# Optimization experiments

Measured on AMD Instinct MI355X. Metric: run time of the kernel, lower is better.

The kernel has to match this reference:

```python
import jax, jax.numpy as jnp
import numpy as np

N, E, H, G = 20000, 320000, 256, 128
FN, FE, OUT = 64, 16, 10
EPS_GEN = 1e-7
EPS_BN = 1e-5
EPS_IN = 1e-5


def _lstm_cell_c(x, W, b):
    # torch LSTMCell with zero (h0, c0); only cell state c' is used:
    # c' = sigmoid(i) * tanh(g).  W: [4H, F], gate order i, f, g, o.
    z = x @ W.T + b
    i, f, g, o = jnp.split(z, 4, axis=1)
    return jax.nn.sigmoid(i) * jnp.tanh(g)


def _segment_softmax(scores, seg, num):
    m = jax.ops.segment_max(scores, seg, num_segments=num)
    m = jnp.where(jnp.isfinite(m), m, 0.0)
    e = jnp.exp(scores - m[seg])
    s = jax.ops.segment_sum(e, seg, num_segments=num)
    return e / (s[seg] + 1e-16)


def _gen_conv(x, src, dst, edge_attr, t, w1, b1, gamma, beta, w2, b2):
    # GENConv (aggr='softmax', t learnable scalar, eps=1e-7, 2-layer MLP)
    msg = jax.nn.relu(x[src] + edge_attr) + EPS_GEN          # [E, H]
    alpha = _segment_softmax(msg * t, dst, N)                 # [E, H]
    aggr = jax.ops.segment_sum(alpha * msg, dst, num_segments=N)  # [N, H]
    h = x + aggr
    h = h @ w1.T + b1                                         # [N, 2H]
    # BatchNorm1d in eval mode (running_mean=0, running_var=1)
    h = h / jnp.sqrt(1.0 + EPS_BN) * gamma + beta
    h = jax.nn.relu(h)
    return h @ w2.T + b2                                      # [N, H]


def _instance_norm(x, batch):
    ones = jnp.ones((x.shape[0],), x.dtype)
    cnt = jnp.maximum(jax.ops.segment_sum(ones, batch, num_segments=G), 1.0)[:, None]
    mean = jax.ops.segment_sum(x, batch, num_segments=G) / cnt
    var = jax.ops.segment_sum(x * x, batch, num_segments=G) / cnt - mean ** 2
    return (x - mean[batch]) / jnp.sqrt(var[batch] + EPS_IN)


def setup_inputs() -> dict:
    key = jax.random.key(0)
    ks = jax.random.split(key, 24)

    def glorot(k, shape):
        lim = 1.0 / np.sqrt(shape[-1])
        return jax.random.uniform(k, shape, jnp.float32, -lim, lim)

    inp = {
        "x": jax.random.normal(ks[0], (N, FN), jnp.float32),
        "edge_index": jax.random.randint(ks[1], (2, E), 0, N),
        "edge_attr": jax.random.normal(ks[2], (E, FE), jnp.float32),
        "batch": jnp.sort(jax.random.randint(ks[3], (N,), 0, G)),
        # LSTMCell embeddings
        "node_W": glorot(ks[4], (4 * H, FN)),
        "node_b": glorot(ks[5], (4 * H,)),
        "edge_W": glorot(ks[6], (4 * H, FE)),
        "edge_b": glorot(ks[7], (4 * H,)),
        # GENConv 1
        "t1": jnp.float32(1.0),
        "g1_w1": glorot(ks[8], (2 * H, H)),
        "g1_b1": glorot(ks[9], (2 * H,)),
        "g1_gamma": jnp.ones((2 * H,), jnp.float32),
        "g1_beta": jnp.zeros((2 * H,), jnp.float32),
        "g1_w2": glorot(ks[10], (H, 2 * H)),
        "g1_b2": glorot(ks[11], (H,)),
        # GENConv 2
        "t2": jnp.float32(1.0),
        "g2_w1": glorot(ks[12], (2 * H, H)),
        "g2_b1": glorot(ks[13], (2 * H,)),
        "g2_gamma": jnp.ones((2 * H,), jnp.float32),
        "g2_beta": jnp.zeros((2 * H,), jnp.float32),
        "g2_w2": glorot(ks[14], (H, 2 * H)),
        "g2_b2": glorot(ks[15], (H,)),
        # output Linear
        "lin_w": glorot(ks[16], (OUT, H)),
        "lin_b": glorot(ks[17], (OUT,)),
    }
    return inp


def reference(x, edge_index, edge_attr, batch,
              node_W, node_b, edge_W, edge_b,
              t1, g1_w1, g1_b1, g1_gamma, g1_beta, g1_w2, g1_b2,
              t2, g2_w1, g2_b1, g2_gamma, g2_beta, g2_w2, g2_b2,
              lin_w, lin_b):
    src, dst = edge_index[0], edge_index[1]
    h = _lstm_cell_c(x, node_W, node_b)            # [N, H]
    ea = _lstm_cell_c(edge_attr, edge_W, edge_b)   # [E, H]
    h = jax.nn.relu(_gen_conv(h, src, dst, ea, t1, g1_w1, g1_b1, g1_gamma, g1_beta, g1_w2, g1_b2))
    h = _instance_norm(h, batch)
    h = jax.nn.relu(_gen_conv(h, src, dst, ea, t2, g2_w1, g2_b1, g2_gamma, g2_beta, g2_w2, g2_b2))
    h = _instance_norm(h, batch)
    pooled = jax.ops.segment_max(h, batch, num_segments=G)  # [G, H]
    pooled = jnp.where(jnp.isfinite(pooled), pooled, 0.0)
    # dropout is identity in eval mode
    out = pooled @ lin_w.T + lin_b
    return jax.nn.sigmoid(out)
```

## Files before the change

### kernel.cpp

```cpp
#include <hip/hip_runtime.h>
#include <hip/hip_bf16.h>
#include <math.h>

#define N_NODES 20000
#define N_EDGES 320000
#define HH      256
#define GG      128
#define FN      64
#define FE      16

__device__ __forceinline__ float fast_rcp(float x) {
    return __builtin_amdgcn_rcpf(x);
}
__device__ __forceinline__ float fast_sigmoid(float x) {
    return fast_rcp(1.f + __expf(-x));
}
__device__ __forceinline__ float sig_tanh(float zi, float zg) {
    float u = __expf(-zi);
    float v = __expf(2.f * zg);
    return (v - 1.f) * fast_rcp((1.f + u) * (v + 1.f));
}

__global__ void hist_k(const int* __restrict__ dst, int* __restrict__ cnt) {
    int e = blockIdx.x * blockDim.x + threadIdx.x;
    if (e < N_EDGES) atomicAdd(&cnt[dst[e]], 1);
}

__global__ __launch_bounds__(256) void scan1_k(const int* __restrict__ cnt,
                                               int* __restrict__ ex,
                                               int* __restrict__ bsum) {
    int b = blockIdx.x, t = threadIdx.x;
    int i = b * 256 + t;
    int v = (i < N_NODES) ? cnt[i] : 0;
    int lane = t & 63, w = t >> 6;
    int incl = v;
#pragma unroll
    for (int off = 1; off < 64; off <<= 1) {
        int u = __shfl_up(incl, off);
        if (lane >= off) incl += u;
    }
    __shared__ int wsum[4];
    if (lane == 63) wsum[w] = incl;
    __syncthreads();
    int woff = 0;
#pragma unroll
    for (int j = 0; j < 4; ++j)
        if (j < w) woff += wsum[j];
    if (i < N_NODES) ex[i] = woff + incl - v;
    if (t == 255) bsum[b] = woff + incl;
}

__global__ __launch_bounds__(128) void scan2_k(int* __restrict__ bsum, int nb) {
    int t = threadIdx.x;
    int v = (t < nb) ? bsum[t] : 0;
    int lane = t & 63, w = t >> 6;
    int incl = v;
#pragma unroll
    for (int off = 1; off < 64; off <<= 1) {
        int u = __shfl_up(incl, off);
        if (lane >= off) incl += u;
    }
    __shared__ int wsum[2];
    if (lane == 63) wsum[w] = incl;
    __syncthreads();
    int woff = (w == 1) ? wsum[0] : 0;
    if (t < nb) bsum[t] = woff + incl - v;
}

__global__ __launch_bounds__(256) void scan3_k(const int* __restrict__ cnt,
                                               const int* __restrict__ bsum,
                                               int* __restrict__ rowst,
                                               int* __restrict__ cursor) {
    int b = blockIdx.x, t = threadIdx.x;
    int i = b * 256 + t;
    if (i < N_NODES) {
        int v = rowst[i] + bsum[b];
        rowst[i] = v;
        cursor[i] = v;
        if (i == N_NODES - 1) rowst[N_NODES] = v + cnt[i];
    }
}

__global__ void scatter_k(const int* __restrict__ src,
                          const int* __restrict__ dst,
                          const float* __restrict__ eattr,
                          int* __restrict__ cursor, int* __restrict__ srcs,
                          float* __restrict__ eattrs) {
    int e = blockIdx.x * blockDim.x + threadIdx.x;
    if (e < N_EDGES) {
        int pos = atomicAdd(&cursor[dst[e]], 1);
        srcs[pos] = src[e];
        const float4* a = (const float4*)(eattr + (size_t)e * FE);
        float4* o = (float4*)(eattrs + (size_t)pos * FE);
        o[0] = a[0];
        o[1] = a[1];
        o[2] = a[2];
        o[3] = a[3];
    }
}

__global__ void repack_k(const float* __restrict__ W, const float* __restrict__ b,
                         float* __restrict__ W2, float* __restrict__ b2, int K) {
    int idx = blockIdx.x * blockDim.x + threadIdx.x;
    if (idx < 512 * K) {
        int r = idx / K, k = idx - r * K;
        int c = r >> 1;
        int rs = (r & 1) ? (512 + c) : c;
        W2[idx] = W[rs * K + k];
    } else if (idx < 512 * K + 512) {
        int r = idx - 512 * K;
        int c = r >> 1;
        int rs = (r & 1) ? (512 + c) : c;
        b2[r] = b[rs];
    }
}

#define NPB 8
__global__ __launch_bounds__(256, 8) void genconv_edge_k(
    const float* __restrict__ hin, const __hip_bfloat16* __restrict__ eacsr,
    const int* __restrict__ srcs, const int* __restrict__ rowst,
    const float* __restrict__ tptr, float* __restrict__ aout) {
    int tid = threadIdx.x;
    float tscale = tptr[0];
    int n0 = blockIdx.x * NPB;
    for (int u = 0; u < NPB; ++u) {
        int n = n0 + u;
        if (n >= N_NODES) break;
        int s0 = rowst[n], s1 = rowst[n + 1];
        float hself = hin[(size_t)n * HH + tid];
        float accE0 = 0.f, accWE0 = 0.f, accE1 = 0.f, accWE1 = 0.f;
        int j = s0;
        for (; j + 1 < s1; j += 2) {
            int sn0 = srcs[j], sn1 = srcs[j + 1];
            float ea0 = __bfloat162float(eacsr[(size_t)j * HH + tid]);
            float ea1 = __bfloat162float(eacsr[(size_t)(j + 1) * HH + tid]);
            float h0v = hin[(size_t)sn0 * HH + tid];
            float h1v = hin[(size_t)sn1 * HH + tid];
            float m0 = fmaxf(h0v + ea0, 0.f) + 1e-7f;
            float m1 = fmaxf(h1v + ea1, 0.f) + 1e-7f;
            float p0 = __expf(tscale * m0);
            float p1 = __expf(tscale * m1);
            accE0 += p0;
            accWE0 += p0 * m0;
            accE1 += p1;
            accWE1 += p1 * m1;
        }
        if (j < s1) {
            int sn = srcs[j];
            float eav = __bfloat162float(eacsr[(size_t)j * HH + tid]);
            float hv = hin[(size_t)sn * HH + tid];
            float m0 = fmaxf(hv + eav, 0.f) + 1e-7f;
            float p0 = __expf(tscale * m0);
            accE0 += p0;
            accWE0 += p0 * m0;
        }
        float accE = accE0 + accE1, accWE = accWE0 + accWE1;
        aout[(size_t)n * HH + tid] = hself + accWE / (accE + 1e-16f);
    }
}

#define TM 128
#define TN 128
#define KB 16
__global__ __launch_bounds__(256, 2) void gemm_nt_k(
    const float* __restrict__ A, const float* __restrict__ B,
    const float* __restrict__ bias, const float* __restrict__ gamma,
    const float* __restrict__ beta, float* __restrict__ C, int M, int NN,
    int K, int mode) {
    __shared__ float As[KB][TM + 4];
    __shared__ float Bs[KB][TN + 4];
    int tid = threadIdx.x;
    int row0 = blockIdx.x * TM, col0 = blockIdx.y * TN;
    int tx = tid & 15, ty = tid >> 4;
    int lr = tid >> 2;
    int lc = (tid & 3) * 4;
    float4 va[2], vb[2];
#pragma unroll
    for (int h = 0; h < 2; ++h) {
        int r = lr + h * 64;
        int gr = row0 + r;
        va[h] = (gr < M) ? *(const float4*)&A[(size_t)gr * K + lc]
                         : make_float4(0.f, 0.f, 0.f, 0.f);
        vb[h] = *(const float4*)&B[(size_t)(col0 + r) * K + lc];
    }
    float acc[8][8] = {{0.f}};
    for (int k0 = 0; k0 < K; k0 += KB) {
#pragma unroll
        for (int h = 0; h < 2; ++h) {
            int r = lr + h * 64;
            As[lc + 0][r] = va[h].x;
            As[lc + 1][r] = va[h].y;
            As[lc + 2][r] = va[h].z;
            As[lc + 3][r] = va[h].w;
            Bs[lc + 0][r] = vb[h].x;
            Bs[lc + 1][r] = vb[h].y;
            Bs[lc + 2][r] = vb[h].z;
            Bs[lc + 3][r] = vb[h].w;
        }
        __syncthreads();
        int k1 = k0 + KB;
        if (k1 < K) {
#pragma unroll
            for (int h = 0; h < 2; ++h) {
                int r = lr + h * 64;
                int gr = row0 + r;
                va[h] = (gr < M)
                            ? *(const float4*)&A[(size_t)gr * K + k1 + lc]
                            : make_float4(0.f, 0.f, 0.f, 0.f);
                vb[h] = *(const float4*)&B[(size_t)(col0 + r) * K + k1 + lc];
            }
        }
#pragma unroll
        for (int k = 0; k < KB; ++k) {
            float4 a0 = *(const float4*)&As[k][ty * 4];
            float4 a1 = *(const float4*)&As[k][64 + ty * 4];
            float4 b0 = *(const float4*)&Bs[k][tx * 4];
            float4 b1 = *(const float4*)&Bs[k][64 + tx * 4];
            float av[8] = {a0.x, a0.y, a0.z, a0.w, a1.x, a1.y, a1.z, a1.w};
            float bv[8] = {b0.x, b0.y, b0.z, b0.w, b1.x, b1.y, b1.z, b1.w};
#pragma unroll
            for (int i = 0; i < 8; ++i)
#pragma unroll
                for (int j = 0; j < 8; ++j) acc[i][j] += av[i] * bv[j];
        }
        __syncthreads();
    }
    const float bn_rs = rsqrtf(1.f + 1e-5f);
#pragma unroll
    for (int gj = 0; gj < 2; ++gj) {
        int nb = col0 + gj * 64 + tx * 4;
        float bs[4], sc[4], sh[4];
#pragma unroll
        for (int j = 0; j < 4; ++j) {
            bs[j] = bias[nb + j];
            if (mode == 0) {
                sc[j] = gamma[nb + j] * bn_rs;
                sh[j] = beta[nb + j];
            }
        }
#pragma unroll
        for (int gi = 0; gi < 2; ++gi) {
#pragma unroll
            for (int i2 = 0; i2 < 4; ++i2) {
                int m = row0 + gi * 64 + ty * 4 + i2;
                if (m >= M) continue;
                int i = gi * 4 + i2;
                float y[4];
#pragma unroll
                for (int j = 0; j < 4; ++j) {
                    float v = acc[i][gj * 4 + j] + bs[j];
                    if (mode == 0) v = v * sc[j] + sh[j];
                    if (mode == 0 || mode == 1) v = fmaxf(v, 0.f);
                    y[j] = v;
                }
                if (mode == 3) {
                    float2 o;
                    o.x = sig_tanh(y[0], y[1]);
                    o.y = sig_tanh(y[2], y[3]);
                    *(float2*)&C[(size_t)m * (NN / 2) + nb / 2] = o;
                } else if (mode == 4) {
                    __hip_bfloat162 o;
                    o.x = __float2bfloat16(sig_tanh(y[0], y[1]));
                    o.y = __float2bfloat16(sig_tanh(y[2], y[3]));
                    *(__hip_bfloat162*)((__hip_bfloat16*)C +
                                        (size_t)m * (NN / 2) + nb / 2) = o;
                } else {
                    float4 o = {y[0], y[1], y[2], y[3]};
                    *(float4*)&C[(size_t)m * NN + nb] = o;
                }
            }
        }
    }
}

__device__ __forceinline__ int lowerb(const int* a, int n, int key) {
    int lo = 0, hi = n;
    while (lo < hi) {
        int mid = (lo + hi) >> 1;
        if (a[mid] < key) lo = mid + 1;
        else hi = mid;
    }
    return lo;
}

__global__ __launch_bounds__(256) void inst_norm_k(
    const float* __restrict__ x, const int* __restrict__ batch,
    float* __restrict__ y) {
    __shared__ int sS, sE;
    int g = blockIdx.x, t = threadIdx.x;
    if (t == 0) {
        sS = lowerb(batch, N_NODES, g);
        sE = lowerb(batch, N_NODES, g + 1);
    }
    __syncthreads();
    int s = sS, e = sE;
    float sum = 0.f, ss = 0.f;
    for (int n = s; n < e; ++n) {
        float v = x[(size_t)n * HH + t];
        sum += v;
        ss += v * v;
    }
    float c = (float)((e - s) > 0 ? (e - s) : 1);
    float mean = sum / c;
    float var = ss / c - mean * mean;
    float inv = rsqrtf(var + 1e-5f);
    for (int n = s; n < e; ++n) {
        float v = x[(size_t)n * HH + t];
        y[(size_t)n * HH + t] = (v - mean) * inv;
    }
}

__global__ __launch_bounds__(256) void inpool_k(
    const float* __restrict__ x, const int* __restrict__ batch,
    const float* __restrict__ lw, const float* __restrict__ lb,
    float* __restrict__ out) {
    __shared__ float pooled[HH];
    __shared__ int sS, sE;
    int g = blockIdx.x, t = threadIdx.x;
    if (t == 0) {
        sS = lowerb(batch, N_NODES, g);
        sE = lowerb(batch, N_NODES, g + 1);
    }
    __syncthreads();
    int s = sS, e = sE;
    float sum = 0.f, ss = 0.f;
    for (int n = s; n < e; ++n) {
        float v = x[(size_t)n * HH + t];
        sum += v;
        ss += v * v;
    }
    float c = (float)((e - s) > 0 ? (e - s) : 1);
    float mean = sum / c;
    float var = ss / c - mean * mean;
    float inv = rsqrtf(var + 1e-5f);
    float m = -3.0e38f;
    for (int n = s; n < e; ++n) {
        float v = (x[(size_t)n * HH + t] - mean) * inv;
        m = fmaxf(m, v);
    }
    pooled[t] = (e > s) ? m : 0.f;
    __syncthreads();
    if (t < 10) {
        float acc = lb[t];
        for (int k = 0; k < HH; ++k) acc += pooled[k] * lw[t * HH + k];
        out[g * 10 + t] = fast_sigmoid(acc);
    }
}

extern "C" void kernel_launch(void* const* d_in, const int* in_sizes, int n_in,
                              void* d_out, int out_size, void* d_ws,
                              size_t ws_size, hipStream_t stream) {
    const float* x      = (const float*)d_in[0];
    const int*   ei     = (const int*)d_in[1];
    const float* eattr  = (const float*)d_in[2];
    const int*   batch  = (const int*)d_in[3];
    const float* nodeW  = (const float*)d_in[4];
    const float* nodeb  = (const float*)d_in[5];
    const float* edgeW  = (const float*)d_in[6];
    const float* edgeb  = (const float*)d_in[7];
    const float* t1     = (const float*)d_in[8];
    const float* g1w1   = (const float*)d_in[9];
    const float* g1b1   = (const float*)d_in[10];
    const float* g1g    = (const float*)d_in[11];
    const float* g1be   = (const float*)d_in[12];
    const float* g1w2   = (const float*)d_in[13];
    const float* g1b2   = (const float*)d_in[14];
    const float* t2     = (const float*)d_in[15];
    const float* g2w1   = (const float*)d_in[16];
    const float* g2b1   = (const float*)d_in[17];
    const float* g2g    = (const float*)d_in[18];
    const float* g2be   = (const float*)d_in[19];
    const float* g2w2   = (const float*)d_in[20];
    const float* g2b2   = (const float*)d_in[21];
    const float* linw   = (const float*)d_in[22];
    const float* linb   = (const float*)d_in[23];
    float* out = (float*)d_out;

    const int* srcA = ei;
    const int* dstA = ei + N_EDGES;

    float* F0  = (float*)d_ws;
    float* F1  = F0 + (size_t)N_NODES * HH;
    float* F2  = F1 + (size_t)N_NODES * HH;
    float* W2n = F2 + (size_t)N_NODES * 2 * HH;
    float* b2n = W2n + 512 * 64;
    float* W2e = b2n + 512;
    float* b2e = W2e + 512 * 16;
    float* eattrs = b2e + 512;
    __hip_bfloat16* eacsr =
        (__hip_bfloat16*)(eattrs + (size_t)N_EDGES * FE);
    int* cnt    = (int*)(eacsr + (size_t)N_EDGES * HH);
    int* cursor = cnt + N_NODES;
    int* rowst  = cursor + N_NODES;
    int* srcs   = rowst + N_NODES + 1;
    int* bsum   = srcs + N_EDGES;

    const int NSCB = (N_NODES + 255) / 256;

    hipMemsetAsync(cnt, 0, N_NODES * sizeof(int), stream);
    hist_k<<<(N_EDGES + 255) / 256, 256, 0, stream>>>(dstA, cnt);
    scan1_k<<<NSCB, 256, 0, stream>>>(cnt, rowst, bsum);
    scan2_k<<<1, 128, 0, stream>>>(bsum, NSCB);
    scan3_k<<<NSCB, 256, 0, stream>>>(cnt, bsum, rowst, cursor);
    scatter_k<<<(N_EDGES + 255) / 256, 256, 0, stream>>>(srcA, dstA, eattr,
                                                         cursor, srcs, eattrs);

    repack_k<<<(512 * 64 + 512 + 255) / 256, 256, 0, stream>>>(nodeW, nodeb,
                                                               W2n, b2n, 64);
    repack_k<<<(512 * 16 + 512 + 255) / 256, 256, 0, stream>>>(edgeW, edgeb,
                                                               W2e, b2e, 16);

    dim3 gemm_grid1((N_NODES + TM - 1) / TM, 512 / TN);
    dim3 gemm_grid2((N_NODES + TM - 1) / TM, 256 / TN);

    gemm_nt_k<<<gemm_grid1, 256, 0, stream>>>(x, W2n, b2n, nullptr, nullptr,
                                              F0, N_NODES, 512, 64, 3);
    gemm_nt_k<<<dim3(N_EDGES / TM, 512 / TN), 256, 0, stream>>>(
        eattrs, W2e, b2e, nullptr, nullptr, (float*)eacsr, N_EDGES, 512, 16, 4);

    genconv_edge_k<<<(N_NODES + NPB - 1) / NPB, 256, 0, stream>>>(
        F0, eacsr, srcs, rowst, t1, F1);
    gemm_nt_k<<<gemm_grid1, 256, 0, stream>>>(F1, g1w1, g1b1, g1g, g1be, F2,
                                              N_NODES, 512, 256, 0);
    gemm_nt_k<<<gemm_grid2, 256, 0, stream>>>(F2, g1w2, g1b2, nullptr, nullptr,
                                              F1, N_NODES, 256, 512, 1);
    inst_norm_k<<<GG, 256, 0, stream>>>(F1, batch, F0);

    genconv_edge_k<<<(N_NODES + NPB - 1) / NPB, 256, 0, stream>>>(
        F0, eacsr, srcs, rowst, t2, F1);
    gemm_nt_k<<<gemm_grid1, 256, 0, stream>>>(F1, g2w1, g2b1, g2g, g2be, F2,
                                              N_NODES, 512, 256, 0);
    gemm_nt_k<<<gemm_grid2, 256, 0, stream>>>(F2, g2w2, g2b2, nullptr, nullptr,
                                              F1, N_NODES, 256, 512, 1);

    inpool_k<<<GG, 256, 0, stream>>>(F1, batch, linw, linb, out);
}
```

Before: 978.7 us.

## Move GENConv MLP and edge LSTM GEMMs to split-bf16 MFMA

```diff
diff --git a/kernel.cpp b/kernel.cpp
--- a/kernel.cpp
+++ b/kernel.cpp
@@ -1,13 +1,16 @@
 #include <hip/hip_runtime.h>
-#include <hip/hip_bf16.h>
 #include <math.h>
 
 #define N_NODES 20000
 #define N_EDGES 320000
 #define HH      256
 #define GG      128
-#define FN      64
 #define FE      16
+#define MPAD    20032
+
+typedef short  bf16x8 __attribute__((ext_vector_type(8)));
+typedef float  f32x4  __attribute__((ext_vector_type(4)));
+typedef unsigned short ushort_t;
 
 __device__ __forceinline__ float fast_rcp(float x) {
     return __builtin_amdgcn_rcpf(x);
@@ -19,6 +22,13 @@
     float u = __expf(-zi);
     float v = __expf(2.f * zg);
     return (v - 1.f) * fast_rcp((1.f + u) * (v + 1.f));
+}
+__device__ __forceinline__ ushort_t f2bf(float x) {
+    unsigned u = __float_as_uint(x);
+    return (ushort_t)((u + 0x7fffu + ((u >> 16) & 1u)) >> 16);
+}
+__device__ __forceinline__ float bf2f(ushort_t h) {
+    return __uint_as_float(((unsigned)h) << 16);
 }
 
 __global__ void hist_k(const int* __restrict__ dst, int* __restrict__ cnt) {
@@ -85,18 +95,35 @@
                           const int* __restrict__ dst,
                           const float* __restrict__ eattr,
                           int* __restrict__ cursor, int* __restrict__ srcs,
-                          float* __restrict__ eattrs) {
+                          ushort_t* __restrict__ eaH,
+                          ushort_t* __restrict__ eaL) {
     int e = blockIdx.x * blockDim.x + threadIdx.x;
-    if (e < N_EDGES) {
-        int pos = atomicAdd(&cursor[dst[e]], 1);
-        srcs[pos] = src[e];
-        const float4* a = (const float4*)(eattr + (size_t)e * FE);
-        float4* o = (float4*)(eattrs + (size_t)pos * FE);
-        o[0] = a[0];
-        o[1] = a[1];
-        o[2] = a[2];
-        o[3] = a[3];
-    }
+    if (e >= N_EDGES) return;
+    int pos = atomicAdd(&cursor[dst[e]], 1);
+    srcs[pos] = src[e];
+    const float4* a4 = (const float4*)(eattr + (size_t)e * FE);
+    float a[16];
+#pragma unroll
+    for (int q = 0; q < 4; ++q) {
+        float4 v = a4[q];
+        a[q * 4 + 0] = v.x; a[q * 4 + 1] = v.y;
+        a[q * 4 + 2] = v.z; a[q * 4 + 3] = v.w;
+    }
+    unsigned hu[8], lu[8];
+#pragma unroll
+    for (int j = 0; j < 8; ++j) {
+        ushort_t h0 = f2bf(a[2 * j]), h1 = f2bf(a[2 * j + 1]);
+        ushort_t l0 = f2bf(a[2 * j] - bf2f(h0));
+        ushort_t l1 = f2bf(a[2 * j + 1] - bf2f(h1));
+        hu[j] = (unsigned)h0 | ((unsigned)h1 << 16);
+        lu[j] = (unsigned)l0 | ((unsigned)l1 << 16);
+    }
+    uint4* ph = (uint4*)(eaH + (size_t)pos * 16);
+    uint4* pl = (uint4*)(eaL + (size_t)pos * 16);
+    ph[0] = make_uint4(hu[0], hu[1], hu[2], hu[3]);
+    ph[1] = make_uint4(hu[4], hu[5], hu[6], hu[7]);
+    pl[0] = make_uint4(lu[0], lu[1], lu[2], lu[3]);
+    pl[1] = make_uint4(lu[4], lu[5], lu[6], lu[7]);
 }
 
 __global__ void repack_k(const float* __restrict__ W, const float* __restrict__ b,
@@ -115,11 +142,138 @@
     }
 }
 
+__global__ void repack_edge_k(const float* __restrict__ W,
+                              ushort_t* __restrict__ Wh,
+                              ushort_t* __restrict__ Wl) {
+    int idx = blockIdx.x * blockDim.x + threadIdx.x;
+    if (idx >= 512 * 16) return;
+    int r = idx >> 4, k = idx & 15;
+    int rs = (r < 256) ? r : (512 + r - 256);
+    float v = W[rs * 16 + k];
+    ushort_t h = f2bf(v);
+    Wh[idx] = h;
+    Wl[idx] = f2bf(v - bf2f(h));
+}
+
+__global__ void convw_k(const float* __restrict__ W, ushort_t* __restrict__ Wh,
+                        ushort_t* __restrict__ Wl, int n) {
+    int i = blockIdx.x * blockDim.x + threadIdx.x;
+    if (i < n) {
+        float x = W[i];
+        ushort_t h = f2bf(x);
+        Wh[i] = h;
+        Wl[i] = f2bf(x - bf2f(h));
+    }
+}
+
+__global__ __launch_bounds__(256, 2) void edge_gemm_k(
+    const ushort_t* __restrict__ Ah, const ushort_t* __restrict__ Al,
+    const ushort_t* __restrict__ Bh, const ushort_t* __restrict__ Bl,
+    const float* __restrict__ eb, ushort_t* __restrict__ eacsr) {
+    int tid = threadIdx.x;
+    int w = tid >> 6, l = tid & 63;
+    int row0 = blockIdx.x * 64 + w * 16;
+    int lr = l & 15, lk = l >> 4;
+    bf16x8 ah = {0, 0, 0, 0, 0, 0, 0, 0};
+    bf16x8 al = {0, 0, 0, 0, 0, 0, 0, 0};
+    if (lk < 2) {
+        ah = *(const bf16x8*)(Ah + (size_t)(row0 + lr) * 16 + lk * 8);
+        al = *(const bf16x8*)(Al + (size_t)(row0 + lr) * 16 + lk * 8);
+    }
+    f32x4 acc[32];
+#pragma unroll
+    for (int i = 0; i < 32; ++i) acc[i] = (f32x4){0.f, 0.f, 0.f, 0.f};
+#pragma unroll
+    for (int ct = 0; ct < 32; ++ct) {
+        bf16x8 bh = {0, 0, 0, 0, 0, 0, 0, 0};
+        bf16x8 bl = {0, 0, 0, 0, 0, 0, 0, 0};
+        if (lk < 2) {
+            bh = *(const bf16x8*)(Bh + (size_t)(ct * 16 + lr) * 16 + lk * 8);
+            bl = *(const bf16x8*)(Bl + (size_t)(ct * 16 + lr) * 16 + lk * 8);
+        }
+        acc[ct] = __builtin_amdgcn_mfma_f32_16x16x32_bf16(ah, bh, acc[ct], 0, 0, 0);
+        acc[ct] = __builtin_amdgcn_mfma_f32_16x16x32_bf16(ah, bl, acc[ct], 0, 0, 0);
+        acc[ct] = __builtin_amdgcn_mfma_f32_16x16x32_bf16(al, bh, acc[ct], 0, 0, 0);
+    }
+#pragma unroll
+    for (int ct = 0; ct < 16; ++ct) {
+        int ci = ct * 16 + lr;
+        float bi = eb[ci], bg = eb[512 + ci];
+#pragma unroll
+        for (int r = 0; r < 4; ++r) {
+            int m = row0 + lk * 4 + r;
+            float zi = acc[ct][r] + bi;
+            float zg = acc[ct + 16][r] + bg;
+            eacsr[(size_t)m * HH + ci] = f2bf(sig_tanh(zi, zg));
+        }
+    }
+}
+
+__global__ __launch_bounds__(256, 2) void gemm_mfma_k(
+    const ushort_t* __restrict__ Ah, const ushort_t* __restrict__ Al,
+    const ushort_t* __restrict__ Bh, const ushort_t* __restrict__ Bl,
+    const float* __restrict__ bias, const float* __restrict__ gamma,
+    const float* __restrict__ beta, ushort_t* __restrict__ Ph,
+    ushort_t* __restrict__ Pl, float* __restrict__ Cf, int M, int NN, int K,
+    int mode) {
+    int tid = threadIdx.x;
+    int w = tid >> 6, l = tid & 63;
+    int row0 = blockIdx.x * 64 + w * 16;
+    int col0 = blockIdx.y * 256;
+    int lr = l & 15, lk = l >> 4;
+    f32x4 acc[16];
+#pragma unroll
+    for (int i = 0; i < 16; ++i) acc[i] = (f32x4){0.f, 0.f, 0.f, 0.f};
+    const ushort_t* arh = Ah + (size_t)(row0 + lr) * K + lk * 8;
+    const ushort_t* arl = Al + (size_t)(row0 + lr) * K + lk * 8;
+    const ushort_t* brh = Bh + (size_t)(col0 + lr) * K + lk * 8;
+    const ushort_t* brl = Bl + (size_t)(col0 + lr) * K + lk * 8;
+    for (int kc = 0; kc < K; kc += 32) {
+        bf16x8 ah = *(const bf16x8*)(arh + kc);
+        bf16x8 al = *(const bf16x8*)(arl + kc);
+#pragma unroll
+        for (int ct = 0; ct < 16; ++ct) {
+            bf16x8 bh = *(const bf16x8*)(brh + (size_t)ct * 16 * K + kc);
+            bf16x8 bl = *(const bf16x8*)(brl + (size_t)ct * 16 * K + kc);
+            acc[ct] = __builtin_amdgcn_mfma_f32_16x16x32_bf16(ah, bh, acc[ct], 0, 0, 0);
+            acc[ct] = __builtin_amdgcn_mfma_f32_16x16x32_bf16(ah, bl, acc[ct], 0, 0, 0);
+            acc[ct] = __builtin_amdgcn_mfma_f32_16x16x32_bf16(al, bh, acc[ct], 0, 0, 0);
+        }
+    }
+    const float bn_rs = rsqrtf(1.f + 1e-5f);
+#pragma unroll
+    for (int ct = 0; ct < 16; ++ct) {
+        int c = col0 + ct * 16 + lr;
+        float bs = bias[c];
+        float sc = 1.f, sh = 0.f;
+        if (mode == 0) {
+            sc = gamma[c] * bn_rs;
+            sh = beta[c];
+        }
+#pragma unroll
+        for (int r = 0; r < 4; ++r) {
+            int m = row0 + lk * 4 + r;
+            if (m >= M) continue;
+            float v = acc[ct][r] + bs;
+            if (mode == 0) v = v * sc + sh;
+            v = fmaxf(v, 0.f);
+            if (mode == 0) {
+                ushort_t h = f2bf(v);
+                Ph[(size_t)m * NN + c] = h;
+                Pl[(size_t)m * NN + c] = f2bf(v - bf2f(h));
+            } else {
+                Cf[(size_t)m * NN + c] = v;
+            }
+        }
+    }
+}
+
 #define NPB 8
 __global__ __launch_bounds__(256, 8) void genconv_edge_k(
-    const float* __restrict__ hin, const __hip_bfloat16* __restrict__ eacsr,
+    const float* __restrict__ hin, const ushort_t* __restrict__ eacsr,
     const int* __restrict__ srcs, const int* __restrict__ rowst,
-    const float* __restrict__ tptr, float* __restrict__ aout) {
+    const float* __restrict__ tptr, ushort_t* __restrict__ Oh,
+    ushort_t* __restrict__ Ol) {
     int tid = threadIdx.x;
     float tscale = tptr[0];
     int n0 = blockIdx.x * NPB;
@@ -132,8 +286,8 @@
         int j = s0;
         for (; j + 1 < s1; j += 2) {
             int sn0 = srcs[j], sn1 = srcs[j + 1];
-            float ea0 = __bfloat162float(eacsr[(size_t)j * HH + tid]);
-            float ea1 = __bfloat162float(eacsr[(size_t)(j + 1) * HH + tid]);
+            float ea0 = bf2f(eacsr[(size_t)j * HH + tid]);
+            float ea1 = bf2f(eacsr[(size_t)(j + 1) * HH + tid]);
             float h0v = hin[(size_t)sn0 * HH + tid];
             float h1v = hin[(size_t)sn1 * HH + tid];
             float m0 = fmaxf(h0v + ea0, 0.f) + 1e-7f;
@@ -147,15 +301,17 @@
         }
         if (j < s1) {
             int sn = srcs[j];
-            float eav = __bfloat162float(eacsr[(size_t)j * HH + tid]);
+            float eav = bf2f(eacsr[(size_t)j * HH + tid]);
             float hv = hin[(size_t)sn * HH + tid];
             float m0 = fmaxf(hv + eav, 0.f) + 1e-7f;
             float p0 = __expf(tscale * m0);
             accE0 += p0;
             accWE0 += p0 * m0;
         }
-        float accE = accE0 + accE1, accWE = accWE0 + accWE1;
-        aout[(size_t)n * HH + tid] = hself + accWE / (accE + 1e-16f);
+        float v = hself + (accWE0 + accWE1) / (accE0 + accE1 + 1e-16f);
+        ushort_t h = f2bf(v);
+        Oh[(size_t)n * HH + tid] = h;
+        Ol[(size_t)n * HH + tid] = f2bf(v - bf2f(h));
     }
 }
 
@@ -164,9 +320,8 @@
 #define KB 16
 __global__ __launch_bounds__(256, 2) void gemm_nt_k(
     const float* __restrict__ A, const float* __restrict__ B,
-    const float* __restrict__ bias, const float* __restrict__ gamma,
-    const float* __restrict__ beta, float* __restrict__ C, int M, int NN,
-    int K, int mode) {
+    const float* __restrict__ bias, float* __restrict__ C, int M, int NN,
+    int K) {
     __shared__ float As[KB][TM + 4];
     __shared__ float Bs[KB][TN + 4];
     int tid = threadIdx.x;
@@ -225,19 +380,12 @@
         }
         __syncthreads();
     }
-    const float bn_rs = rsqrtf(1.f + 1e-5f);
 #pragma unroll
     for (int gj = 0; gj < 2; ++gj) {
         int nb = col0 + gj * 64 + tx * 4;
-        float bs[4], sc[4], sh[4];
-#pragma unroll
-        for (int j = 0; j < 4; ++j) {
-            bs[j] = bias[nb + j];
-            if (mode == 0) {
-                sc[j] = gamma[nb + j] * bn_rs;
-                sh[j] = beta[nb + j];
-            }
-        }
+        float bs[4];
+#pragma unroll
+        for (int j = 0; j < 4; ++j) bs[j] = bias[nb + j];
 #pragma unroll
         for (int gi = 0; gi < 2; ++gi) {
 #pragma unroll
@@ -245,29 +393,14 @@
                 int m = row0 + gi * 64 + ty * 4 + i2;
                 if (m >= M) continue;
                 int i = gi * 4 + i2;
-                float y[4];
-#pragma unroll
-                for (int j = 0; j < 4; ++j) {
-                    float v = acc[i][gj * 4 + j] + bs[j];
-                    if (mode == 0) v = v * sc[j] + sh[j];
-                    if (mode == 0 || mode == 1) v = fmaxf(v, 0.f);
-                    y[j] = v;
-                }
-                if (mode == 3) {
-                    float2 o;
-                    o.x = sig_tanh(y[0], y[1]);
-                    o.y = sig_tanh(y[2], y[3]);
-                    *(float2*)&C[(size_t)m * (NN / 2) + nb / 2] = o;
-                } else if (mode == 4) {
-                    __hip_bfloat162 o;
-                    o.x = __float2bfloat16(sig_tanh(y[0], y[1]));
-                    o.y = __float2bfloat16(sig_tanh(y[2], y[3]));
-                    *(__hip_bfloat162*)((__hip_bfloat16*)C +
-                                        (size_t)m * (NN / 2) + nb / 2) = o;
-                } else {
-                    float4 o = {y[0], y[1], y[2], y[3]};
-                    *(float4*)&C[(size_t)m * NN + nb] = o;
-                }
+                float y0 = acc[i][gj * 4 + 0] + bs[0];
+                float y1 = acc[i][gj * 4 + 1] + bs[1];
+                float y2 = acc[i][gj * 4 + 2] + bs[2];
+                float y3 = acc[i][gj * 4 + 3] + bs[3];
+                float2 o;
+                o.x = sig_tanh(y0, y1);
+                o.y = sig_tanh(y2, y3);
+                *(float2*)&C[(size_t)m * (NN / 2) + nb / 2] = o;
             }
         }
     }
@@ -379,21 +512,45 @@
     const int* srcA = ei;
     const int* dstA = ei + N_EDGES;
 
-    float* F0  = (float*)d_ws;
-    float* F1  = F0 + (size_t)N_NODES * HH;
-    float* F2  = F1 + (size_t)N_NODES * HH;
-    float* W2n = F2 + (size_t)N_NODES * 2 * HH;
-    float* b2n = W2n + 512 * 64;
-    float* W2e = b2n + 512;
-    float* b2e = W2e + 512 * 16;
-    float* eattrs = b2e + 512;
-    __hip_bfloat16* eacsr =
-        (__hip_bfloat16*)(eattrs + (size_t)N_EDGES * FE);
-    int* cnt    = (int*)(eacsr + (size_t)N_EDGES * HH);
-    int* cursor = cnt + N_NODES;
-    int* rowst  = cursor + N_NODES;
-    int* srcs   = rowst + N_NODES + 1;
-    int* bsum   = srcs + N_EDGES;
+    auto AL = [](size_t b) { return (b + 255) & ~(size_t)255; };
+    char* p = (char*)d_ws;
+    float* F0 = (float*)p;
+    p += AL((size_t)N_NODES * HH * 4);
+    char* EA = p;
+    ushort_t* eaH = (ushort_t*)EA;
+    ushort_t* eaL = (ushort_t*)(EA + AL((size_t)N_EDGES * 16 * 2));
+    ushort_t* F1h = (ushort_t*)EA;
+    ushort_t* F1l = (ushort_t*)(EA + AL((size_t)MPAD * HH * 2));
+    float* F1f = (float*)EA;
+    size_t sp1 = 2 * AL((size_t)N_EDGES * 16 * 2);
+    size_t sp2 = 2 * AL((size_t)MPAD * HH * 2);
+    size_t sp3 = AL((size_t)N_NODES * HH * 4);
+    size_t spm = sp1 > sp2 ? sp1 : sp2;
+    if (sp3 > spm) spm = sp3;
+    p += AL(spm);
+    ushort_t* F2h = (ushort_t*)p;
+    p += AL((size_t)MPAD * 512 * 2);
+    ushort_t* F2l = (ushort_t*)p;
+    p += AL((size_t)MPAD * 512 * 2);
+    ushort_t* eacsr = (ushort_t*)p;
+    p += AL((size_t)N_EDGES * HH * 2);
+    ushort_t* w11h = (ushort_t*)p; p += AL(512 * 256 * 2);
+    ushort_t* w11l = (ushort_t*)p; p += AL(512 * 256 * 2);
+    ushort_t* w12h = (ushort_t*)p; p += AL(256 * 512 * 2);
+    ushort_t* w12l = (ushort_t*)p; p += AL(256 * 512 * 2);
+    ushort_t* w21h = (ushort_t*)p; p += AL(512 * 256 * 2);
+    ushort_t* w21l = (ushort_t*)p; p += AL(512 * 256 * 2);
+    ushort_t* w22h = (ushort_t*)p; p += AL(256 * 512 * 2);
+    ushort_t* w22l = (ushort_t*)p; p += AL(256 * 512 * 2);
+    ushort_t* weh  = (ushort_t*)p; p += AL(512 * 16 * 2);
+    ushort_t* wel  = (ushort_t*)p; p += AL(512 * 16 * 2);
+    float* W2n = (float*)p; p += AL(512 * 64 * 4);
+    float* b2n = (float*)p; p += AL(512 * 4);
+    int* cnt    = (int*)p; p += AL((size_t)N_NODES * 4);
+    int* cursor = (int*)p; p += AL((size_t)N_NODES * 4);
+    int* rowst  = (int*)p; p += AL(((size_t)N_NODES + 1) * 4);
+    int* srcs   = (int*)p; p += AL((size_t)N_EDGES * 4);
+    int* bsum   = (int*)p; p += AL(128 * 4);
 
     const int NSCB = (N_NODES + 255) / 256;
 
@@ -403,35 +560,43 @@
     scan2_k<<<1, 128, 0, stream>>>(bsum, NSCB);
     scan3_k<<<NSCB, 256, 0, stream>>>(cnt, bsum, rowst, cursor);
     scatter_k<<<(N_EDGES + 255) / 256, 256, 0, stream>>>(srcA, dstA, eattr,
-                                                         cursor, srcs, eattrs);
+                                                         cursor, srcs, eaH, eaL);
 
     repack_k<<<(512 * 64 + 512 + 255) / 256, 256, 0, stream>>>(nodeW, nodeb,
                                                                W2n, b2n, 64);
-    repack_k<<<(512 * 16 + 512 + 255) / 256, 256, 0, stream>>>(edgeW, edgeb,
-                                                               W2e, b2e, 16);
-
-    dim3 gemm_grid1((N_NODES + TM - 1) / TM, 512 / TN);
-    dim3 gemm_grid2((N_NODES + TM - 1) / TM, 256 / TN);
-
-    gemm_nt_k<<<gemm_grid1, 256, 0, stream>>>(x, W2n, b2n, nullptr, nullptr,
-                                              F0, N_NODES, 512, 64, 3);
-    gemm_nt_k<<<dim3(N_EDGES / TM, 512 / TN), 256, 0, stream>>>(
-        eattrs, W2e, b2e, nullptr, nullptr, (float*)eacsr, N_EDGES, 512, 16, 4);
+    repack_edge_k<<<(512 * 16 + 255) / 256, 256, 0, stream>>>(edgeW, weh, wel);
+    convw_k<<<512, 256, 0, stream>>>(g1w1, w11h, w11l, 512 * 256);
+    convw_k<<<512, 256, 0, stream>>>(g1w2, w12h, w12l, 256 * 512);
+    convw_k<<<512, 256, 0, stream>>>(g2w1, w21h, w21l, 512 * 256);
+    convw_k<<<512, 256, 0, stream>>>(g2w2, w22h, w22l, 256 * 512);
+
+    edge_gemm_k<<<N_EDGES / 64, 256, 0, stream>>>(eaH, eaL, weh, wel, edgeb,
+                                                  eacsr);
+
+    gemm_nt_k<<<dim3((N_NODES + TM - 1) / TM, 512 / TN), 256, 0, stream>>>(
+        x, W2n, b2n, F0, N_NODES, 512, 64);
+
+    dim3 g1grid((N_NODES + 63) / 64, 2);
+    dim3 g2grid((N_NODES + 63) / 64, 1);
 
     genconv_edge_k<<<(N_NODES + NPB - 1) / NPB, 256, 0, stream>>>(
-        F0, eacsr, srcs, rowst, t1, F1);
-    gemm_nt_k<<<gemm_grid1, 256, 0, stream>>>(F1, g1w1, g1b1, g1g, g1be, F2,
-                                              N_NODES, 512, 256, 0);
-    gemm_nt_k<<<gemm_grid2, 256, 0, stream>>>(F2, g1w2, g1b2, nullptr, nullptr,
-                                              F1, N_NODES, 256, 512, 1);
-    inst_norm_k<<<GG, 256, 0, stream>>>(F1, batch, F0);
+        F0, eacsr, srcs, rowst, t1, F1h, F1l);
+    gemm_mfma_k<<<g1grid, 256, 0, stream>>>(F1h, F1l, w11h, w11l, g1b1, g1g,
+                                            g1be, F2h, F2l, nullptr, N_NODES,
+                                            512, 256, 0);
+    gemm_mfma_k<<<g2grid, 256, 0, stream>>>(F2h, F2l, w12h, w12l, g1b2, g1b2,
+                                            g1b2, nullptr, nullptr, F1f,
+                                            N_NODES, 256, 512, 1);
+    inst_norm_k<<<GG, 256, 0, stream>>>(F1f, batch, F0);
 
     genconv_edge_k<<<(N_NODES + NPB - 1) / NPB, 256, 0, stream>>>(
-        F0, eacsr, srcs, rowst, t2, F1);
-    gemm_nt_k<<<gemm_grid1, 256, 0, stream>>>(F1, g2w1, g2b1, g2g, g2be, F2,
-                                              N_NODES, 512, 256, 0);
-    gemm_nt_k<<<gemm_grid2, 256, 0, stream>>>(F2, g2w2, g2b2, nullptr, nullptr,
-                                              F1, N_NODES, 256, 512, 1);
-
-    inpool_k<<<GG, 256, 0, stream>>>(F1, batch, linw, linb, out);
-}
+        F0, eacsr, srcs, rowst, t2, F1h, F1l);
+    gemm_mfma_k<<<g1grid, 256, 0, stream>>>(F1h, F1l, w21h, w21l, g2b1, g2g,
+                                            g2be, F2h, F2l, nullptr, N_NODES,
+                                            512, 256, 0);
+    gemm_mfma_k<<<g2grid, 256, 0, stream>>>(F2h, F2l, w22h, w22l, g2b2, g2b2,
+                                            g2b2, nullptr, nullptr, F1f,
+                                            N_NODES, 256, 512, 1);
+
+    inpool_k<<<GG, 256, 0, stream>>>(F1f, batch, linw, linb, out);
+}
```

New measurement: 1.066 ms. 1.09x slower.
